# Optimization experiments

Measured on AMD Instinct MI355X. Metric: run time of the kernel, lower is better.

The kernel has to match this reference:

```python
import jax, jax.numpy as jnp
import numpy as np

N_NODES = 8192
N_EDGES = 131072
BATCH = 2
HID = 256      # hidden_dim
MSG = 256      # message_dim
EDIM = 64      # edge feature dim
MLP_H = 512    # message MLP hidden width
OUT = 128      # readout dim
N_ITERS = 3


def setup_inputs() -> dict:
    key = jax.random.key(0)
    ks = jax.random.split(key, 20)
    s = 0.05  # small init so iterated GRU stays well-conditioned
    inp = {
        "edge_feat": jax.random.normal(ks[0], (N_EDGES, BATCH, EDIM), jnp.float32),
        "W1": jax.random.normal(ks[1], (HID + HID + EDIM, MLP_H), jnp.float32) * s,
        "b1": jnp.zeros((MLP_H,), jnp.float32),
        "W2": jax.random.normal(ks[2], (MLP_H, MSG), jnp.float32) * s,
        "b2": jnp.zeros((MSG,), jnp.float32),
        "Wr": jax.random.normal(ks[3], (MSG, HID), jnp.float32) * s,
        "Ur": jax.random.normal(ks[4], (HID, HID), jnp.float32) * s,
        "br": jnp.zeros((HID,), jnp.float32),
        "Wz": jax.random.normal(ks[5], (MSG, HID), jnp.float32) * s,
        "Uz": jax.random.normal(ks[6], (HID, HID), jnp.float32) * s,
        "bz": jnp.zeros((HID,), jnp.float32),
        "Wh": jax.random.normal(ks[7], (MSG, HID), jnp.float32) * s,
        "Uh": jax.random.normal(ks[8], (HID, HID), jnp.float32) * s,
        "bh": jnp.zeros((HID,), jnp.float32),
        "Wo": jax.random.normal(ks[9], (HID, OUT), jnp.float32) * s,
        "bo": jnp.zeros((OUT,), jnp.float32),
        "edge_src": jax.random.randint(ks[10], (N_EDGES,), 0, N_NODES, jnp.int32),
        "edge_dst": jax.random.randint(ks[11], (N_EDGES,), 0, N_NODES, jnp.int32),
    }
    return inp


def reference(edge_feat, W1, b1, W2, b2, Wr, Ur, br, Wz, Uz, bz,
              Wh, Uh, bh, Wo, bo, edge_src, edge_dst):
    # reset_hidden_states: zeros for hidden and persistent message accumulator
    h = jnp.zeros((N_NODES, BATCH, HID), edge_feat.dtype)
    m = jnp.zeros((N_NODES, BATCH, MSG), edge_feat.dtype)

    for _ in range(N_ITERS):
        # gather endpoint hiddens: h_v = receiver (dst), h_w = sender (src)
        h_v = h[edge_dst]                       # [E, B, HID]
        h_w = h[edge_src]                       # [E, B, HID]
        x = jnp.concatenate([h_v, h_w, edge_feat], axis=-1)  # [E, B, 576]
        # per-edge message MLP
        msg = jax.nn.relu(x @ W1 + b1) @ W2 + b2              # [E, B, MSG]
        # scatter-sum into receiving nodes; accumulator persists across iters
        m = m + jax.ops.segment_sum(msg, edge_dst, num_segments=N_NODES)
        # GRU vertex update: h = GRU(m, h)
        r = jax.nn.sigmoid(m @ Wr + h @ Ur + br)
        z = jax.nn.sigmoid(m @ Wz + h @ Uz + bz)
        h_tilde = jnp.tanh(m @ Wh + (r * h) @ Uh + bh)
        h = (1.0 - z) * h + z * h_tilde

    # readout: sum node hiddens, then linear
    g = jnp.sum(h, axis=0)                      # [B, HID]
    return g @ Wo + bo                          # [B, OUT]
```

## Files before the change

### kernel.cpp

```cpp
#include <hip/hip_runtime.h>
#include <hip/hip_bf16.h>

#define E_EDGES 131072
#define NNODES  8192
#define NB      16384
#define HID     256
#define EDIM    64
#define MLPH    512
#define OUTD    128
#define NIT     3
#define RB      32

typedef short s16x4 __attribute__((ext_vector_type(4)));
typedef short s16x8 __attribute__((ext_vector_type(8)));
typedef float f32x4 __attribute__((ext_vector_type(4)));
typedef float f32x2 __attribute__((ext_vector_type(2)));

__device__ __forceinline__ short f2bf(float f){
  unsigned int x = __builtin_bit_cast(unsigned int, f);
  x += 0x7fffu + ((x >> 16) & 1u);
  return (short)(x >> 16);
}
__device__ __forceinline__ float bf2f(short s){
  unsigned int x = ((unsigned int)(unsigned short)s) << 16;
  return __builtin_bit_cast(float, x);
}
__device__ __forceinline__ void gload_lds16(const void* g, void* l){
  __builtin_amdgcn_global_load_lds(
      (const __attribute__((address_space(1))) void*)g,
      (__attribute__((address_space(3))) void*)l, 16, 0, 0);
}
#define MFMA16(a,b,c) __builtin_amdgcn_mfma_f32_16x16x32_bf16((a),(b),(c),0,0,0)

#if defined(__has_builtin)
#if __has_builtin(__builtin_amdgcn_cvt_pk_f32_fp8) && __has_builtin(__builtin_amdgcn_cvt_pk_fp8_f32)
#define FP8_HW 1
#endif
#endif
#ifndef FP8_HW
#define FP8_HW 0
#endif

__device__ __forceinline__ unsigned char enc_fp8_sw(float f){
  unsigned int b = __builtin_bit_cast(unsigned int, f);
  unsigned int s = (b >> 24) & 0x80u;
  float a = fabsf(f);
  if (a >= 448.f) return (unsigned char)(s | 0x7e);
  if (a < 0.015625f){
    int q = (int)rintf(a * 512.f);
    return (unsigned char)(s | (unsigned int)q);
  }
  unsigned int e32  = (b >> 23) & 0xff;
  unsigned int mant = b & 0x7fffff;
  unsigned int rnd  = mant + 0x7ffff + ((mant >> 20) & 1);
  unsigned int e8   = e32 - 120 + (rnd >> 23);
  unsigned int m3   = (rnd >> 20) & 7;
  if (e8 >= 16) return (unsigned char)(s | 0x7e);
  return (unsigned char)(s | (e8 << 3) | m3);
}
__device__ __forceinline__ float dec_fp8_sw(unsigned int v){
  unsigned int s = (v >> 7) & 1, e = (v >> 3) & 15, m = v & 7;
  float r;
  if (e == 0) r = (float)m * 0.001953125f;
  else        r = __builtin_bit_cast(float, ((e + 120u) << 23) | (m << 20));
  return s ? -r : r;
}
__device__ __forceinline__ unsigned char enc_fp8(float f){
#if FP8_HW
  unsigned int pk = (unsigned int)__builtin_amdgcn_cvt_pk_fp8_f32(f, f, 0, false);
  return (unsigned char)(pk & 0xff);
#else
  return enc_fp8_sw(f);
#endif
}
__device__ __forceinline__ void dec_fp8x4(unsigned int ev, float& e0, float& e1,
                                          float& e2, float& e3){
#if FP8_HW
  f32x2 lo = __builtin_amdgcn_cvt_pk_f32_fp8((int)ev, false);
  f32x2 hi = __builtin_amdgcn_cvt_pk_f32_fp8((int)ev, true);
  e0 = lo[0]; e1 = lo[1]; e2 = hi[0]; e3 = hi[1];
#else
  e0 = dec_fp8_sw(ev & 0xff); e1 = dec_fp8_sw((ev >> 8) & 0xff);
  e2 = dec_fp8_sw((ev >> 16) & 0xff); e3 = dec_fp8_sw(ev >> 24);
#endif
}

__global__ __launch_bounds__(256, 4)
void e1_gemm(const float* __restrict__ ef, const short* __restrict__ BtE,
             unsigned char* __restrict__ E1, const float* __restrict__ b1,
             const int* __restrict__ ceid)
{
  __shared__ __align__(16) short As[128 * 64];
  __shared__ __align__(16) short Bs[128 * 64];

  const int t  = threadIdx.x;
  const int w  = t >> 6, l = t & 63;
  const int lr = l & 15, lg = l >> 4;
  const int wr = w >> 1, wc = w & 1;
  const int browbase = blockIdx.x * 128;
  const int bcolbase = blockIdx.y * 128;
  const int srow = t >> 3;
  const int scol = (t & 7) * 8;

#pragma unroll
  for (int i = 0; i < 4; ++i)
    gload_lds16(BtE + (size_t)(bcolbase + srow + i * 32) * 64 + scol,
                (char*)Bs + w * 1024 + i * 4096);

#pragma unroll
  for (int i = 0; i < 4; ++i){
    int R = browbase + srow + i * 32;
    int e = ceid[R >> 1];
    const float* ap = ef + ((size_t)e * 2 + (R & 1)) * EDIM + scol;
    f32x4 f0 = *(const f32x4*)ap;
    f32x4 f1 = *(const f32x4*)(ap + 4);
    s16x8 o;
    o[0]=f2bf(f0[0]); o[1]=f2bf(f0[1]); o[2]=f2bf(f0[2]); o[3]=f2bf(f0[3]);
    o[4]=f2bf(f1[0]); o[5]=f2bf(f1[1]); o[6]=f2bf(f1[2]); o[7]=f2bf(f1[3]);
    int row = srow + i * 32;
    *(s16x8*)(As + row * 64 + (scol ^ ((row & 7) << 3))) = o;
  }
  __syncthreads();

  f32x4 acc[4][4];
#pragma unroll
  for (int mf = 0; mf < 4; ++mf)
#pragma unroll
    for (int e2 = 0; e2 < 4; ++e2) acc[mf][e2] = (f32x4){0.f,0.f,0.f,0.f};

#pragma unroll
  for (int kk = 0; kk < 2; ++kk){
    s16x8 a[4], b[4];
#pragma unroll
    for (int e2 = 0; e2 < 4; ++e2){
      int ar = wr*64 + e2*16 + lr;
      a[e2] = *(const s16x8*)(As + ar * 64 + ((kk*32 + lg*8) ^ ((ar & 7) << 3)));
    }
#pragma unroll
    for (int mf = 0; mf < 4; ++mf){
      int br = wc*64 + mf*16 + lr;
      b[mf] = *(const s16x8*)(Bs + br * 64 + ((kk*32 + lg*8) ^ ((br & 7) << 3)));
    }
#pragma unroll
    for (int mf = 0; mf < 4; ++mf)
#pragma unroll
      for (int e2 = 0; e2 < 4; ++e2)
        acc[mf][e2] = MFMA16(b[mf], a[e2], acc[mf][e2]);
  }
#pragma unroll
  for (int mf = 0; mf < 4; ++mf){
    int mcol0 = bcolbase + wc*64 + mf*16 + lg*4;
    f32x4 bv = *(const f32x4*)(b1 + mcol0);
#pragma unroll
    for (int e2 = 0; e2 < 4; ++e2){
      int erow = browbase + wr*64 + e2*16 + lr;
      unsigned int pk = (unsigned int)enc_fp8(acc[mf][e2][0] + bv[0])
                      | ((unsigned int)enc_fp8(acc[mf][e2][1] + bv[1]) << 8)
                      | ((unsigned int)enc_fp8(acc[mf][e2][2] + bv[2]) << 16)
                      | ((unsigned int)enc_fp8(acc[mf][e2][3] + bv[3]) << 24);
      *(unsigned int*)(E1 + (size_t)erow * MLPH + mcol0) = pk;
    }
  }
}

template<bool USE_P>
__global__ __launch_bounds__(256)
void edge_kernel(const short* __restrict__ P, const unsigned char* __restrict__ E1,
                 const int* __restrict__ csr_src, const int* __restrict__ row_start,
                 short* __restrict__ S)
{
  const int n = blockIdx.x;
  const int t = threadIdx.x;
  const int b = t >> 7;
  const int j = (t & 127) << 2;
  const int ps = row_start[n], pe = row_start[n + 1];

  float p10 = 0.f, p11 = 0.f, p12 = 0.f, p13 = 0.f;
  if (USE_P){
    s16x4 t1 = *(const s16x4*)(P + (size_t)(n * 2 + b) * 1024 + j);
    p10 = bf2f(t1[0]); p11 = bf2f(t1[1]); p12 = bf2f(t1[2]); p13 = bf2f(t1[3]);
  }
  float a0 = 0.f, a1 = 0.f, a2 = 0.f, a3 = 0.f;
  for (int p = ps; p < pe; ++p){
    unsigned int ev = *(const unsigned int*)(E1 + ((size_t)p * 2 + b) * 512 + j);
    float e0, e1, e2, e3;
    dec_fp8x4(ev, e0, e1, e2, e3);
    float x0 = p10 + e0, x1 = p11 + e1, x2 = p12 + e2, x3 = p13 + e3;
    if (USE_P){
      int src = csr_src[p];
      s16x4 v2 = *(const s16x4*)(P + (size_t)(src * 2 + b) * 1024 + 512 + j);
      x0 += bf2f(v2[0]); x1 += bf2f(v2[1]); x2 += bf2f(v2[2]); x3 += bf2f(v2[3]);
    }
    a0 += fmaxf(x0, 0.f); a1 += fmaxf(x1, 0.f);
    a2 += fmaxf(x2, 0.f); a3 += fmaxf(x3, 0.f);
  }
  s16x4 o; o[0] = f2bf(a0); o[1] = f2bf(a1); o[2] = f2bf(a2); o[3] = f2bf(a3);
  *(s16x4*)(S + (size_t)(n * 2 + b) * 512 + j) = o;
}

template<int PH>
__global__ __launch_bounds__(512, 4)
void node_update(const short* __restrict__ S, short* __restrict__ Pout,
                 float* __restrict__ m, float* __restrict__ h,
                 float* __restrict__ g,
                 const short* __restrict__ BtW2, const short* __restrict__ BtRZ,
                 const short* __restrict__ BtHW, const short* __restrict__ BtP,
                 const int* __restrict__ deg, const float* __restrict__ b2,
                 const float* __restrict__ br, const float* __restrict__ bz,
                 const float* __restrict__ bh)
{
  __shared__ __align__(16) char lds[69632];
  short* As = (short*)lds;
  short* Bs = (short*)(lds + 4096);
  short* Ms = (short*)(lds + 36864);
  short* Xs = (short*)(lds + 53248);
  float* Hf = (float*)lds;

  const int tid = threadIdx.x;
  const int w = tid >> 6, l = tid & 63;
  const int lr = l & 15, lg = l >> 4;
  const int wq = w >> 2, wc = w & 3;
  const int grow0 = blockIdx.x * RB;

  auto stageB = [&](const short* Bt, int K, int pcol0, int k0){
#pragma unroll
    for (int i = 0; i < 4; ++i){
      int u = i * 512 + tid;
      int row = u >> 3, uc = u & 7;
      const short* gp = Bt + (size_t)(pcol0 + row) * K + k0 + ((uc ^ (row & 7)) << 3);
      gload_lds16(gp, (char*)Bs + i * 8192 + w * 1024);
    }
  };
  auto stageA_S = [&](int k0){
    if (w < 4){
      int u = w * 64 + l;
      int row = u >> 3, uc = u & 7;
      const short* gp = S + (size_t)(grow0 + row) * 512 + k0 + ((uc ^ (row & 7)) << 3);
      gload_lds16(gp, (char*)As + w * 1024);
    }
  };
  auto rdA64 = [&](int row, int colel){ return row * 64 + (colel ^ ((row & 7) << 3)); };
  auto rd256 = [&](int row, int colel){ return row * 256 + (colel ^ ((row & 7) << 3)); };

  f32x4 hv[4], acc[4];
#pragma unroll
  for (int j = 0; j < 4; ++j)
#pragma unroll
    for (int r = 0; r < 4; ++r){
      int rl = wq*16 + lg*4 + r, colp = wc*64 + j*16 + lr;
      size_t gi = (size_t)(grow0 + rl) * 256 + colp;
      float base = (float)deg[(grow0 + rl) >> 1] * b2[colp];
      if (PH > 0){ base += m[gi]; hv[j][r] = h[gi]; }
      else hv[j][r] = 0.f;
      acc[j][r] = base;
    }
  if (PH > 0){
#pragma unroll
    for (int j = 0; j < 4; ++j)
#pragma unroll
      for (int r = 0; r < 4; ++r){
        int rl = wq*16 + lg*4 + r, colp = wc*64 + j*16 + lr;
        Xs[rd256(rl, colp)] = f2bf(hv[j][r]);
      }
  }

  for (int c = 0; c < 8; ++c){
    __syncthreads();
    stageA_S(c * 64);
    stageB(BtW2, 512, 0, c * 64);
    __syncthreads();
#pragma unroll
    for (int kk = 0; kk < 2; ++kk){
      s16x8 a0 = *(const s16x8*)(As + rdA64(wq*16 + lr, kk*32 + lg*8));
#pragma unroll
      for (int j = 0; j < 4; ++j){
        s16x8 bb = *(const s16x8*)(Bs + rdA64(wc*64 + j*16 + lr, kk*32 + lg*8));
        acc[j] = MFMA16(a0, bb, acc[j]);
      }
    }
  }
#pragma unroll
  for (int j = 0; j < 4; ++j)
#pragma unroll
    for (int r = 0; r < 4; ++r){
      int rl = wq*16 + lg*4 + r, colp = wc*64 + j*16 + lr;
      float v = acc[j][r];
      if (PH < 2) m[(size_t)(grow0 + rl) * 256 + colp] = v;
      Ms[rd256(rl, colp)] = f2bf(v);
    }

  const int NC = (PH > 0) ? 8 : 4;

  f32x4 Gr[4], Gz[4];
#pragma unroll
  for (int j = 0; j < 4; ++j){ Gr[j] = (f32x4){0.f,0.f,0.f,0.f}; Gz[j] = (f32x4){0.f,0.f,0.f,0.f}; }

  for (int c = 0; c < NC; ++c){
    __syncthreads();
    stageB(BtRZ, 512, 0, c * 64);
    __syncthreads();
    const short* Ab = (c < 4) ? Ms : Xs;
    int kb = (c & 3) * 64;
#pragma unroll
    for (int kk = 0; kk < 2; ++kk){
      s16x8 a0 = *(const s16x8*)(Ab + rd256(wq*16 + lr, kb + kk*32 + lg*8));
#pragma unroll
      for (int j = 0; j < 4; ++j){
        s16x8 bb = *(const s16x8*)(Bs + rdA64(wc*64 + j*16 + lr, kk*32 + lg*8));
        Gr[j] = MFMA16(a0, bb, Gr[j]);
      }
    }
  }
  for (int c = 0; c < NC; ++c){
    __syncthreads();
    stageB(BtRZ, 512, 256, c * 64);
    __syncthreads();
    const short* Ab = (c < 4) ? Ms : Xs;
    int kb = (c & 3) * 64;
#pragma unroll
    for (int kk = 0; kk < 2; ++kk){
      s16x8 a0 = *(const s16x8*)(Ab + rd256(wq*16 + lr, kb + kk*32 + lg*8));
#pragma unroll
      for (int j = 0; j < 4; ++j){
        s16x8 bb = *(const s16x8*)(Bs + rdA64(wc*64 + j*16 + lr, kk*32 + lg*8));
        Gz[j] = MFMA16(a0, bb, Gz[j]);
      }
    }
  }

  f32x4 zz[4];
#pragma unroll
  for (int j = 0; j < 4; ++j)
#pragma unroll
    for (int r = 0; r < 4; ++r){
      int colp = wc*64 + j*16 + lr;
      zz[j][r] = 1.f / (1.f + __expf(-(Gz[j][r] + bz[colp])));
    }
  if (PH > 0){
    __syncthreads();
#pragma unroll
    for (int j = 0; j < 4; ++j)
#pragma unroll
      for (int r = 0; r < 4; ++r){
        int rl = wq*16 + lg*4 + r, colp = wc*64 + j*16 + lr;
        float rr = 1.f / (1.f + __expf(-(Gr[j][r] + br[colp])));
        Xs[rd256(rl, colp)] = f2bf(rr * hv[j][r]);
      }
    __syncthreads();
  }

  f32x4 Gw[4];
#pragma unroll
  for (int j = 0; j < 4; ++j) Gw[j] = (f32x4){0.f,0.f,0.f,0.f};
  for (int c = 0; c < NC; ++c){
    __syncthreads();
    stageB(BtHW, 512, 0, c * 64);
    __syncthreads();
    const short* Ab = (c < 4) ? Ms : Xs;
    int kb = (c & 3) * 64;
#pragma unroll
    for (int kk = 0; kk < 2; ++kk){
      s16x8 a0 = *(const s16x8*)(Ab + rd256(wq*16 + lr, kb + kk*32 + lg*8));
#pragma unroll
      for (int j = 0; j < 4; ++j){
        s16x8 bb = *(const s16x8*)(Bs + rdA64(wc*64 + j*16 + lr, kk*32 + lg*8));
        Gw[j] = MFMA16(a0, bb, Gw[j]);
      }
    }
  }

  __syncthreads();
#pragma unroll
  for (int j = 0; j < 4; ++j)
#pragma unroll
    for (int r = 0; r < 4; ++r){
      int rl = wq*16 + lg*4 + r, colp = wc*64 + j*16 + lr;
      float ht = tanhf(Gw[j][r] + bh[colp]);
      float z  = zz[j][r];
      float hn = (1.f - z) * hv[j][r] + z * ht;
      if (PH < 2){
        h[(size_t)(grow0 + rl) * 256 + colp] = hn;
        Ms[rd256(rl, colp)] = f2bf(hn);
      } else {
        Hf[rl * 256 + colp] = hn;
      }
    }
  __syncthreads();

  if (PH < 2){
    for (int pn = 0; pn < 4; ++pn){
      f32x4 pa[4];
#pragma unroll
      for (int j = 0; j < 4; ++j) pa[j] = (f32x4){0.f,0.f,0.f,0.f};
      for (int c = 0; c < 4; ++c){
        __syncthreads();
        stageB(BtP, 256, pn * 256, c * 64);
        __syncthreads();
#pragma unroll
        for (int kk = 0; kk < 2; ++kk){
          s16x8 a0 = *(const s16x8*)(Ms + rd256(wq*16 + lr, c*64 + kk*32 + lg*8));
#pragma unroll
          for (int j = 0; j < 4; ++j){
            s16x8 bb = *(const s16x8*)(Bs + rdA64(wc*64 + j*16 + lr, kk*32 + lg*8));
            pa[j] = MFMA16(a0, bb, pa[j]);
          }
        }
      }
#pragma unroll
      for (int j = 0; j < 4; ++j)
#pragma unroll
        for (int r = 0; r < 4; ++r){
          int colp = wc*64 + j*16 + lr;
          Pout[(size_t)(grow0 + wq*16 + lg*4 + r) * 1024 + pn*256 + colp] = f2bf(pa[j][r]);
        }
    }
  } else {
    int col = tid & 255, pb = (tid >> 8) & 1;
    float s = 0.f;
#pragma unroll
    for (int rr = 0; rr < 16; ++rr)
      s += Hf[(2*rr + pb) * 256 + col];
    atomicAdd(&g[pb * 256 + col], s);
  }
}

__global__ void count_kernel(const int* __restrict__ edst, int* __restrict__ counts){
  int e = blockIdx.x * 256 + threadIdx.x;
  if (e < E_EDGES) atomicAdd(&counts[edst[e]], 1);
}
__global__ void scan_kernel(const int* __restrict__ counts, int* __restrict__ row_start,
                            int* __restrict__ cursor){
  __shared__ int sums[1024];
  int t = threadIdx.x;
  int base = t * 8;
  int loc[8]; int s = 0;
#pragma unroll
  for (int i = 0; i < 8; ++i){ loc[i] = s; s += counts[base + i]; }
  sums[t] = s;
  __syncthreads();
  for (int o = 1; o < 1024; o <<= 1){
    int v = sums[t];
    int u = (t >= o) ? sums[t - o] : 0;
    __syncthreads();
    sums[t] = v + u;
    __syncthreads();
  }
  int excl = (t == 0) ? 0 : sums[t - 1];
#pragma unroll
  for (int i = 0; i < 8; ++i){ int v = excl + loc[i]; row_start[base + i] = v; cursor[base + i] = v; }
  if (t == 1023) row_start[NNODES] = sums[1023];
}
__global__ void fill_kernel(const int* __restrict__ edst, const int* __restrict__ esrc,
                            int* __restrict__ cursor, int* __restrict__ csr_eid,
                            int* __restrict__ csr_src){
  int e = blockIdx.x * 256 + threadIdx.x;
  if (e < E_EDGES){
    int pos = atomicAdd(&cursor[edst[e]], 1);
    csr_eid[pos] = e;
    csr_src[pos] = esrc[e];
  }
}

__global__ void prep_weights(const float* __restrict__ W1, const float* __restrict__ W2,
                             const float* __restrict__ Wr, const float* __restrict__ Ur,
                             const float* __restrict__ Wz, const float* __restrict__ Uz,
                             const float* __restrict__ Wh, const float* __restrict__ Uh,
                             short* __restrict__ BtP, short* __restrict__ BtE,
                             short* __restrict__ BtW2, short* __restrict__ BtRZ,
                             short* __restrict__ BtHW)
{
  int id = blockIdx.x * 256 + threadIdx.x;
  if (id < 262144){
    int jj = id >> 8, k = id & 255;
    float v = (jj < 512) ? W1[(size_t)k * 512 + jj] : W1[(size_t)(256 + k) * 512 + (jj - 512)];
    BtP[id] = f2bf(v);
  } else if (id < 294912){
    int i2 = id - 262144; int jj = i2 >> 6, c = i2 & 63;
    BtE[jj * 64 + (c ^ ((jj & 7) << 3))] = f2bf(W1[(size_t)(512 + c) * 512 + jj]);
  } else if (id < 425984){
    int i2 = id - 294912; int n = i2 >> 9, k = i2 & 511;
    BtW2[i2] = f2bf(W2[(size_t)k * 256 + n]);
  } else if (id < 688128){
    int i2 = id - 425984; int col = i2 >> 9, k = i2 & 511;
    float v;
    if (col < 256) v = (k < 256) ? Wr[(size_t)k * 256 + col] : Ur[(size_t)(k - 256) * 256 + col];
    else { int c2 = col - 256; v = (k < 256) ? Wz[(size_t)k * 256 + c2] : Uz[(size_t)(k - 256) * 256 + c2]; }
    BtRZ[i2] = f2bf(v);
  } else if (id < 819200){
    int i2 = id - 688128; int col = i2 >> 9, k = i2 & 511;
    float v = (k < 256) ? Wh[(size_t)k * 256 + col] : Uh[(size_t)(k - 256) * 256 + col];
    BtHW[i2] = f2bf(v);
  }
}

__global__ __launch_bounds__(256)
void readout2(const float* __restrict__ g, const float* __restrict__ Wo,
              const float* __restrict__ bo, float* __restrict__ out){
  int t = threadIdx.x;
  int b = t >> 7, o = t & 127;
  float s = bo[o];
  for (int c = 0; c < 256; ++c) s += g[b * 256 + c] * Wo[c * 128 + o];
  out[b * 128 + o] = s;
}

extern "C" void kernel_launch(void* const* d_in, const int* in_sizes, int n_in,
                              void* d_out, int out_size, void* d_ws, size_t ws_size,
                              hipStream_t stream)
{
  const float* ef  = (const float*)d_in[0];
  const float* W1  = (const float*)d_in[1];
  const float* b1  = (const float*)d_in[2];
  const float* W2  = (const float*)d_in[3];
  const float* b2  = (const float*)d_in[4];
  const float* Wr  = (const float*)d_in[5];
  const float* Ur  = (const float*)d_in[6];
  const float* br  = (const float*)d_in[7];
  const float* Wz  = (const float*)d_in[8];
  const float* Uz  = (const float*)d_in[9];
  const float* bz  = (const float*)d_in[10];
  const float* Wh  = (const float*)d_in[11];
  const float* Uh  = (const float*)d_in[12];
  const float* bh  = (const float*)d_in[13];
  const float* Wo  = (const float*)d_in[14];
  const float* bo  = (const float*)d_in[15];
  const int* esrc  = (const int*)d_in[16];
  const int* edst  = (const int*)d_in[17];

  char* base = (char*)d_ws;
  size_t off = 0;
  auto alloc = [&](size_t bytes) -> char* {
    off = (off + 255) & ~(size_t)255;
    char* p = base + off;
    off += bytes;
    return p;
  };
  float* h    = (float*)alloc((size_t)NB * 256 * 4);
  float* m    = (float*)alloc((size_t)NB * 256 * 4);
  short* P    = (short*)alloc((size_t)NB * 1024 * 2);
  short* S    = (short*)alloc((size_t)NB * 512 * 2);
  unsigned char* E1 = (unsigned char*)alloc((size_t)E_EDGES * 2 * MLPH);
  short* BtP  = (short*)alloc(262144 * 2);
  short* BtE  = (short*)alloc(32768 * 2);
  short* BtW2 = (short*)alloc(131072 * 2);
  short* BtRZ = (short*)alloc(262144 * 2);
  short* BtHW = (short*)alloc(131072 * 2);
  int* counts = (int*)alloc(NNODES * 4);
  int* rs     = (int*)alloc((NNODES + 1) * 4);
  int* cursor = (int*)alloc(NNODES * 4);
  int* ceid   = (int*)alloc(E_EDGES * 4);
  int* csrc   = (int*)alloc(E_EDGES * 4);
  float* g    = (float*)alloc(512 * 4);

  dim3 blk(256);

  hipMemsetAsync(g,  0, 512 * 4, stream);
  hipMemsetAsync(counts, 0, NNODES * 4, stream);
  prep_weights<<<3200, blk, 0, stream>>>(W1, W2, Wr, Ur, Wz, Uz, Wh, Uh,
                                         BtP, BtE, BtW2, BtRZ, BtHW);
  count_kernel<<<512, blk, 0, stream>>>(edst, counts);
  scan_kernel<<<1, 1024, 0, stream>>>(counts, rs, cursor);
  fill_kernel<<<512, blk, 0, stream>>>(edst, esrc, cursor, ceid, csrc);

  e1_gemm<<<dim3(E_EDGES * 2 / 128, MLPH / 128), blk, 0, stream>>>(
      ef, BtE, E1, b1, ceid);

  edge_kernel<false><<<NNODES, blk, 0, stream>>>(P, E1, csrc, rs, S);
  node_update<0><<<NB / RB, dim3(512), 0, stream>>>(S, P, m, h, g,
      BtW2, BtRZ, BtHW, BtP, counts, b2, br, bz, bh);

  edge_kernel<true><<<NNODES, blk, 0, stream>>>(P, E1, csrc, rs, S);
  node_update<1><<<NB / RB, dim3(512), 0, stream>>>(S, P, m, h, g,
      BtW2, BtRZ, BtHW, BtP, counts, b2, br, bz, bh);

  edge_kernel<true><<<NNODES, blk, 0, stream>>>(P, E1, csrc, rs, S);
  node_update<2><<<NB / RB, dim3(512), 0, stream>>>(S, P, m, h, g,
      BtW2, BtRZ, BtHW, BtP, counts, b2, br, bz, bh);

  readout2<<<1, blk, 0, stream>>>(g, Wo, bo, (float*)d_out);
}
```

Before: 461.3 us.

## Reuse gathered edge-feature tile across all output panels in e1_gemm

The e1_gemm grid drops its column dimension. Each block now gathers and converts its 128-row edge-feature tile once, then loops over the four 128-wide column panels of W1's edge part, reloading only the B tile each time. Before, every block re-gathered and re-converted the same fp32 rows once per panel. The fp8 results are also staged through a swizzled LDS buffer so each thread writes 16-byte coalesced rows instead of scattered 4-byte stores. In exchange there are fewer blocks, less parallelism, more LDS use and an extra barrier per panel, and the occupancy hint drops from 4 to 3.

Result: faster. 419.7 us, median of 2 (-9.0%).

```diff
diff --git a/kernel.cpp b/kernel.cpp
--- a/kernel.cpp
+++ b/kernel.cpp
@@ -15,6 +15,7 @@
 typedef short s16x8 __attribute__((ext_vector_type(8)));
 typedef float f32x4 __attribute__((ext_vector_type(4)));
 typedef float f32x2 __attribute__((ext_vector_type(2)));
+typedef unsigned int u32x4 __attribute__((ext_vector_type(4)));
 
 __device__ __forceinline__ short f2bf(float f){
   unsigned int x = __builtin_bit_cast(unsigned int, f);
@@ -85,27 +86,22 @@
 #endif
 }
 
-__global__ __launch_bounds__(256, 4)
+__global__ __launch_bounds__(256, 3)
 void e1_gemm(const float* __restrict__ ef, const short* __restrict__ BtE,
              unsigned char* __restrict__ E1, const float* __restrict__ b1,
              const int* __restrict__ ceid)
 {
   __shared__ __align__(16) short As[128 * 64];
   __shared__ __align__(16) short Bs[128 * 64];
+  __shared__ __align__(16) unsigned char Ts[128 * 128];
 
   const int t  = threadIdx.x;
   const int w  = t >> 6, l = t & 63;
   const int lr = l & 15, lg = l >> 4;
   const int wr = w >> 1, wc = w & 1;
   const int browbase = blockIdx.x * 128;
-  const int bcolbase = blockIdx.y * 128;
   const int srow = t >> 3;
   const int scol = (t & 7) * 8;
-
-#pragma unroll
-  for (int i = 0; i < 4; ++i)
-    gload_lds16(BtE + (size_t)(bcolbase + srow + i * 32) * 64 + scol,
-                (char*)Bs + w * 1024 + i * 4096);
 
 #pragma unroll
   for (int i = 0; i < 4; ++i){
@@ -120,45 +116,66 @@
     int row = srow + i * 32;
     *(s16x8*)(As + row * 64 + (scol ^ ((row & 7) << 3))) = o;
   }
-  __syncthreads();
-
-  f32x4 acc[4][4];
-#pragma unroll
-  for (int mf = 0; mf < 4; ++mf)
-#pragma unroll
-    for (int e2 = 0; e2 < 4; ++e2) acc[mf][e2] = (f32x4){0.f,0.f,0.f,0.f};
-
-#pragma unroll
-  for (int kk = 0; kk < 2; ++kk){
-    s16x8 a[4], b[4];
-#pragma unroll
-    for (int e2 = 0; e2 < 4; ++e2){
-      int ar = wr*64 + e2*16 + lr;
-      a[e2] = *(const s16x8*)(As + ar * 64 + ((kk*32 + lg*8) ^ ((ar & 7) << 3)));
-    }
+
+  for (int pn = 0; pn < 4; ++pn){
+#pragma unroll
+    for (int i = 0; i < 4; ++i)
+      gload_lds16(BtE + (size_t)(pn * 128 + srow + i * 32) * 64 + scol,
+                  (char*)Bs + w * 1024 + i * 4096);
+    __syncthreads();
+
+    f32x4 acc[4][4];
+#pragma unroll
+    for (int mf = 0; mf < 4; ++mf)
+#pragma unroll
+      for (int e2 = 0; e2 < 4; ++e2) acc[mf][e2] = (f32x4){0.f,0.f,0.f,0.f};
+
+#pragma unroll
+    for (int kk = 0; kk < 2; ++kk){
+      s16x8 a[4], b[4];
+#pragma unroll
+      for (int e2 = 0; e2 < 4; ++e2){
+        int ar = wr*64 + e2*16 + lr;
+        a[e2] = *(const s16x8*)(As + ar * 64 + ((kk*32 + lg*8) ^ ((ar & 7) << 3)));
+      }
+#pragma unroll
+      for (int mf = 0; mf < 4; ++mf){
+        int br = wc*64 + mf*16 + lr;
+        b[mf] = *(const s16x8*)(Bs + br * 64 + ((kk*32 + lg*8) ^ ((br & 7) << 3)));
+      }
+#pragma unroll
+      for (int mf = 0; mf < 4; ++mf)
+#pragma unroll
+        for (int e2 = 0; e2 < 4; ++e2)
+          acc[mf][e2] = MFMA16(b[mf], a[e2], acc[mf][e2]);
+    }
+
 #pragma unroll
     for (int mf = 0; mf < 4; ++mf){
-      int br = wc*64 + mf*16 + lr;
-      b[mf] = *(const s16x8*)(Bs + br * 64 + ((kk*32 + lg*8) ^ ((br & 7) << 3)));
-    }
-#pragma unroll
-    for (int mf = 0; mf < 4; ++mf)
-#pragma unroll
-      for (int e2 = 0; e2 < 4; ++e2)
-        acc[mf][e2] = MFMA16(b[mf], a[e2], acc[mf][e2]);
-  }
-#pragma unroll
-  for (int mf = 0; mf < 4; ++mf){
-    int mcol0 = bcolbase + wc*64 + mf*16 + lg*4;
-    f32x4 bv = *(const f32x4*)(b1 + mcol0);
-#pragma unroll
-    for (int e2 = 0; e2 < 4; ++e2){
-      int erow = browbase + wr*64 + e2*16 + lr;
-      unsigned int pk = (unsigned int)enc_fp8(acc[mf][e2][0] + bv[0])
-                      | ((unsigned int)enc_fp8(acc[mf][e2][1] + bv[1]) << 8)
-                      | ((unsigned int)enc_fp8(acc[mf][e2][2] + bv[2]) << 16)
-                      | ((unsigned int)enc_fp8(acc[mf][e2][3] + bv[3]) << 24);
-      *(unsigned int*)(E1 + (size_t)erow * MLPH + mcol0) = pk;
+      int mloc = wc*64 + mf*16 + lg*4;
+      f32x4 bv = *(const f32x4*)(b1 + pn*128 + mloc);
+      int u = mloc >> 2;
+      int usw_hi = (u >> 2), ulo = (u & 3) << 2;
+#pragma unroll
+      for (int e2 = 0; e2 < 4; ++e2){
+        int erow = wr*64 + e2*16 + lr;
+        unsigned int pk = (unsigned int)enc_fp8(acc[mf][e2][0] + bv[0])
+                        | ((unsigned int)enc_fp8(acc[mf][e2][1] + bv[1]) << 8)
+                        | ((unsigned int)enc_fp8(acc[mf][e2][2] + bv[2]) << 16)
+                        | ((unsigned int)enc_fp8(acc[mf][e2][3] + bv[3]) << 24);
+        *(unsigned int*)(Ts + erow * 128 + ((usw_hi ^ (erow & 7)) << 4) + ulo) = pk;
+      }
+    }
+    __syncthreads();
+
+    {
+      int rr = t >> 1, hh = t & 1;
+#pragma unroll
+      for (int q = 0; q < 4; ++q){
+        int u16 = q * 2 + hh;
+        u32x4 v = *(const u32x4*)(Ts + rr * 128 + ((u16 ^ (rr & 7)) << 4));
+        *(u32x4*)(E1 + (size_t)(browbase + rr) * 512 + pn * 128 + u16 * 16) = v;
+      }
     }
   }
 }
@@ -561,8 +578,7 @@
   scan_kernel<<<1, 1024, 0, stream>>>(counts, rs, cursor);
   fill_kernel<<<512, blk, 0, stream>>>(edst, esrc, cursor, ceid, csrc);
 
-  e1_gemm<<<dim3(E_EDGES * 2 / 128, MLPH / 128), blk, 0, stream>>>(
-      ef, BtE, E1, b1, ceid);
+  e1_gemm<<<E_EDGES * 2 / 128, blk, 0, stream>>>(ef, BtE, E1, b1, ceid);
 
   edge_kernel<false><<<NNODES, blk, 0, stream>>>(P, E1, csrc, rs, S);
   node_update<0><<<NB / RB, dim3(512), 0, stream>>>(S, P, m, h, g,
```
